# Kernel tuning notes

Measured on AMD Instinct MI355X. Metric: run time of the kernel, lower is better.

Reference implementation:

```python
import jax, jax.numpy as jnp
import numpy as np

H = 2048            # hidden_size
IN = 64             # input_size
EMB = 8             # EMBEDDING_DIMS
LIN = IN - 4 + 4 * EMB  # 92, LSTM input width
NH = 13             # number of prediction heads
MAXO = 9            # max head output width (gear)
HEAD_OUTS = [5, 1, 1, 1, 1, 1, 1, 1, 9, 1, 3, 1, 1]
LN_EPS = 1e-5


def setup_inputs() -> dict:
    key = jax.random.key(0)
    ks = jax.random.split(key, 22)
    s = 1.0 / np.sqrt(H)
    d = {}
    d["lap_cont"] = jax.random.normal(ks[0], (1, 1, IN - 4), jnp.float32)
    d["idx"] = jax.random.randint(ks[1], (1, 1, 4), 0, 5)  # compound, driver, track, team
    d["h_s"] = 0.1 * jax.random.normal(ks[2], (2, 1, H), jnp.float32)
    d["c_s"] = 0.1 * jax.random.normal(ks[3], (2, 1, H), jnp.float32)
    d["emb_team"] = 0.02 * jax.random.normal(ks[4], (10, EMB), jnp.float32)
    d["emb_track"] = 0.02 * jax.random.normal(ks[5], (48, EMB), jnp.float32)
    d["emb_driver"] = 0.02 * jax.random.normal(ks[6], (46, EMB), jnp.float32)
    d["emb_compound"] = 0.02 * jax.random.normal(ks[7], (5, EMB), jnp.float32)
    d["W_ih0"] = s * jax.random.normal(ks[8], (4 * H, LIN), jnp.float32)
    d["W_hh0"] = s * jax.random.normal(ks[9], (4 * H, H), jnp.float32)
    d["b_ih0"] = s * jax.random.normal(ks[10], (4 * H,), jnp.float32)
    d["b_hh0"] = s * jax.random.normal(ks[11], (4 * H,), jnp.float32)
    d["W_ih1"] = s * jax.random.normal(ks[12], (4 * H, H), jnp.float32)
    d["W_hh1"] = s * jax.random.normal(ks[13], (4 * H, H), jnp.float32)
    d["b_ih1"] = s * jax.random.normal(ks[14], (4 * H,), jnp.float32)
    d["b_hh1"] = s * jax.random.normal(ks[15], (4 * H,), jnp.float32)
    d["ln_g"] = jnp.ones((H,), jnp.float32)
    d["ln_b"] = jnp.zeros((H,), jnp.float32)
    d["head_W1"] = 0.02 * jax.random.normal(ks[16], (NH, 64, H), jnp.float32)
    d["head_b1"] = 0.02 * jax.random.normal(ks[17], (NH, 64), jnp.float32)
    d["head_W2"] = 0.02 * jax.random.normal(ks[18], (NH, MAXO, 64), jnp.float32)  # padded to MAXO
    d["head_b2"] = 0.02 * jax.random.normal(ks[19], (NH, MAXO), jnp.float32)
    return d


def _lstm_cell(x, h, c, Wih, Whh, bih, bhh):
    # x:[1,in], h,c:[1,H]; PyTorch gate order i,f,g,o
    g = x @ Wih.T + bih + h @ Whh.T + bhh
    i, f, gg, o = jnp.split(g, 4, axis=-1)
    c_new = jax.nn.sigmoid(f) * c + jax.nn.sigmoid(i) * jnp.tanh(gg)
    h_new = jax.nn.sigmoid(o) * jnp.tanh(c_new)
    return h_new, c_new


def reference(lap_cont, idx, h_s, c_s, emb_team, emb_track, emb_driver, emb_compound,
              W_ih0, W_hh0, b_ih0, b_hh0, W_ih1, W_hh1, b_ih1, b_hh1,
              ln_g, ln_b, head_W1, head_b1, head_W2, head_b2):
    # Embeddings (idx order: compound, driver, track_status, team)
    comp_e = emb_compound[idx[:, :, 0]]
    drv_e = emb_driver[idx[:, :, 1]]
    trk_e = emb_track[idx[:, :, 2]]
    team_e = emb_team[idx[:, :, 3]]
    x = jnp.concatenate([lap_cont, team_e, trk_e, drv_e, comp_e], axis=-1)  # [1,1,LIN]

    x2 = x[0]  # seq_len=1 -> single cell step; [1,LIN]
    h0, c0 = _lstm_cell(x2, h_s[0], c_s[0], W_ih0, W_hh0, b_ih0, b_hh0)
    h1, c1 = _lstm_cell(h0, h_s[1], c_s[1], W_ih1, W_hh1, b_ih1, b_hh1)
    new_h = jnp.stack([h0, h1], axis=0)
    new_c = jnp.stack([c0, c1], axis=0)

    h_t = h1[None]  # [1,1,H]
    mu = jnp.mean(h_t, axis=-1, keepdims=True)
    var = jnp.mean(jnp.square(h_t - mu), axis=-1, keepdims=True)
    h_t = (h_t - mu) * jax.lax.rsqrt(var + LN_EPS) * ln_g + ln_b

    # All 13 heads fused: Dropout is identity at inference
    hid = jax.nn.relu(jnp.einsum('bsh,koh->bsko', h_t, head_W1) + head_b1)  # [1,1,13,64]
    outs = jnp.einsum('bsko,kpo->bskp', hid, head_W2) + head_b2              # [1,1,13,9]

    heads = [outs[:, :, k, :HEAD_OUTS[k]] for k in range(NH)]
    return (new_h, new_c, *heads)
```

## Files before the change

### kernel.cpp

```cpp
#include <hip/hip_runtime.h>
#include <hip/hip_bf16.h>

#define H 2048
#define LIN 92

typedef __hip_bfloat16 bf16;

__device__ __align__(16) float g_x[96];
__device__ __align__(16) float g_hs[2][H];
__device__ __align__(16) float g_cs[2][H];
__device__ __align__(16) float g_p1[4 * H];
__device__ __align__(16) float g_h0[H];
__device__ __align__(16) float g_h1[H];
__device__ __align__(16) float g_ht[H];
__device__ __align__(16) float g_hid[13 * 64];

__device__ __forceinline__ float b2f(bf16 v) { return __bfloat162float(v); }
__device__ __forceinline__ float sg(float x) { return 1.f / (1.f + __expf(-x)); }

__device__ __forceinline__ bool is_bf16(const void* ln_g) {
    return *reinterpret_cast<const unsigned*>(ln_g) == 0x3F803F80u;
}

__device__ __forceinline__ float ld(const void* p, long i, bool bf) {
    return bf ? b2f(((const bf16*)p)[i]) : ((const float*)p)[i];
}

struct F8 { float v[8]; };

__device__ __forceinline__ F8 load8bf(const bf16* p) {
    uint4 u = *reinterpret_cast<const uint4*>(p);
    F8 r;
    r.v[0] = __uint_as_float(u.x << 16); r.v[1] = __uint_as_float(u.x & 0xffff0000u);
    r.v[2] = __uint_as_float(u.y << 16); r.v[3] = __uint_as_float(u.y & 0xffff0000u);
    r.v[4] = __uint_as_float(u.z << 16); r.v[5] = __uint_as_float(u.z & 0xffff0000u);
    r.v[6] = __uint_as_float(u.w << 16); r.v[7] = __uint_as_float(u.w & 0xffff0000u);
    return r;
}

__device__ __forceinline__ float wred(float x) {
    #pragma unroll
    for (int o = 32; o > 0; o >>= 1) x += __shfl_down(x, o);
    return x;
}

__device__ __forceinline__ float dotw(const void* W, long rowoff, const float* vec,
                                      int lane, bool bf) {
    float acc = 0.f;
    if (bf) {
        const bf16* r = (const bf16*)W + rowoff;
        #pragma unroll
        for (int i = 0; i < 4; i++) {
            int col = i * 512 + lane * 8;
            F8 a = load8bf(r + col);
            const float4* hp = reinterpret_cast<const float4*>(vec + col);
            float4 h0 = hp[0], h1 = hp[1];
            acc = fmaf(a.v[0], h0.x, acc); acc = fmaf(a.v[1], h0.y, acc);
            acc = fmaf(a.v[2], h0.z, acc); acc = fmaf(a.v[3], h0.w, acc);
            acc = fmaf(a.v[4], h1.x, acc); acc = fmaf(a.v[5], h1.y, acc);
            acc = fmaf(a.v[6], h1.z, acc); acc = fmaf(a.v[7], h1.w, acc);
        }
    } else {
        const float* r = (const float*)W + rowoff;
        #pragma unroll
        for (int i = 0; i < 4; i++) {
            int col = i * 512 + lane * 8;
            const float4* ap = reinterpret_cast<const float4*>(r + col);
            const float4* hp = reinterpret_cast<const float4*>(vec + col);
            float4 a0 = ap[0], a1 = ap[1];
            float4 h0 = hp[0], h1 = hp[1];
            acc = fmaf(a0.x, h0.x, acc); acc = fmaf(a0.y, h0.y, acc);
            acc = fmaf(a0.z, h0.z, acc); acc = fmaf(a0.w, h0.w, acc);
            acc = fmaf(a1.x, h1.x, acc); acc = fmaf(a1.y, h1.y, acc);
            acc = fmaf(a1.z, h1.z, acc); acc = fmaf(a1.w, h1.w, acc);
        }
    }
    return acc;
}

__global__ __launch_bounds__(256) void k_prep(
    const void* __restrict__ lap, const int* __restrict__ idx,
    const void* __restrict__ h_s, const void* __restrict__ c_s,
    const void* __restrict__ e_team, const void* __restrict__ e_trk,
    const void* __restrict__ e_drv, const void* __restrict__ e_cmp,
    const void* __restrict__ ln_g)
{
    bool bf = is_bf16(ln_g);
    int tid = threadIdx.x;
    for (int i = tid; i < H; i += 256) {
        g_hs[0][i] = ld(h_s, i, bf);
        g_hs[1][i] = ld(h_s, H + i, bf);
        g_cs[0][i] = ld(c_s, i, bf);
        g_cs[1][i] = ld(c_s, H + i, bf);
    }
    if (tid < LIN) {
        float v;
        if (tid < 60)      v = ld(lap, tid, bf);
        else if (tid < 68) v = ld(e_team, idx[3] * 8 + tid - 60, bf);
        else if (tid < 76) v = ld(e_trk,  idx[2] * 8 + tid - 68, bf);
        else if (tid < 84) v = ld(e_drv,  idx[1] * 8 + tid - 76, bf);
        else               v = ld(e_cmp,  idx[0] * 8 + tid - 84, bf);
        g_x[tid] = v;
    }
}

__global__ __launch_bounds__(256) void k_phaseA(
    const void* __restrict__ Wih0, const void* __restrict__ Whh0,
    const void* __restrict__ bih0, const void* __restrict__ bhh0,
    const void* __restrict__ Whh1, const void* __restrict__ bih1,
    const void* __restrict__ bhh1, const void* __restrict__ ln_g,
    float* __restrict__ out)
{
    bool bf = is_bf16(ln_g);
    int tid = threadIdx.x, w = tid >> 6, lane = tid & 63;
    if (blockIdx.x < H) {
        int j = blockIdx.x;
        __shared__ float gsh[4];
        long row = j + (long)w * H;
        float acc = 0.f;
        if (lane < 46) {
            long o = row * LIN + lane * 2;
            acc = g_x[lane * 2] * ld(Wih0, o, bf) + g_x[lane * 2 + 1] * ld(Wih0, o + 1, bf);
        }
        acc += dotw(Whh0, row * H, g_hs[0], lane, bf);
        acc = wred(acc);
        if (lane == 0) gsh[w] = acc + ld(bih0, row, bf) + ld(bhh0, row, bf);
        __syncthreads();
        if (tid == 0) {
            float gi = gsh[0], gf = gsh[1], gg = gsh[2], go = gsh[3];
            float cp = g_cs[0][j];
            float cn = sg(gf) * cp + sg(gi) * tanhf(gg);
            float hn = sg(go) * tanhf(cn);
            out[j]         = hn;
            out[2 * H + j] = cn;
            g_h0[j] = hn;
        }
    } else {
        long row = (long)(blockIdx.x - H) * 4 + w;
        float acc = dotw(Whh1, row * H, g_hs[1], lane, bf);
        acc = wred(acc);
        if (lane == 0) g_p1[row] = acc + ld(bih1, row, bf) + ld(bhh1, row, bf);
    }
}

__global__ __launch_bounds__(256) void k_lstm1(
    const void* __restrict__ Wih1, const void* __restrict__ ln_g,
    float* __restrict__ out)
{
    bool bf = is_bf16(ln_g);
    int tid = threadIdx.x, w = tid >> 6, lane = tid & 63;
    int j = blockIdx.x;
    long row = j + (long)w * H;
    float acc = dotw(Wih1, row * H, g_h0, lane, bf);
    acc = wred(acc);
    __shared__ float gsh[4];
    if (lane == 0) gsh[w] = acc + g_p1[row];
    __syncthreads();
    if (tid == 0) {
        float gi = gsh[0], gf = gsh[1], gg = gsh[2], go = gsh[3];
        float cp = g_cs[1][j];
        float cn = sg(gf) * cp + sg(gi) * tanhf(gg);
        float hn = sg(go) * tanhf(cn);
        out[H + j]     = hn;
        out[3 * H + j] = cn;
        g_h1[j] = hn;
    }
}

__global__ __launch_bounds__(256) void k_ln(
    const void* __restrict__ g, const void* __restrict__ b)
{
    bool bf = is_bf16(g);
    int tid = threadIdx.x, w = tid >> 6, lane = tid & 63;
    float vals[8];
    float s = 0.f, s2 = 0.f;
    #pragma unroll
    for (int i = 0; i < 8; i++) {
        float v = g_h1[tid + i * 256];
        vals[i] = v; s += v; s2 += v * v;
    }
    s = wred(s); s2 = wred(s2);
    __shared__ float sh[8];
    __shared__ float mv[2];
    if (lane == 0) { sh[w] = s; sh[4 + w] = s2; }
    __syncthreads();
    if (tid == 0) {
        float ts = sh[0] + sh[1] + sh[2] + sh[3];
        float t2 = sh[4] + sh[5] + sh[6] + sh[7];
        float mu = ts / (float)H;
        float var = t2 / (float)H - mu * mu;
        mv[0] = mu; mv[1] = rsqrtf(var + 1e-5f);
    }
    __syncthreads();
    float mu = mv[0], rs = mv[1];
    #pragma unroll
    for (int i = 0; i < 8; i++) {
        int e = tid + i * 256;
        g_ht[e] = (vals[i] - mu) * rs * ld(g, e, bf) + ld(b, e, bf);
    }
}

__global__ __launch_bounds__(256) void k_head1(
    const void* __restrict__ W1, const void* __restrict__ b1,
    const void* __restrict__ ln_g)
{
    bool bf = is_bf16(ln_g);
    int tid = threadIdx.x, w = tid >> 6, lane = tid & 63;
    int k = blockIdx.x >> 4, o = (blockIdx.x & 15) * 4 + w;
    float acc = dotw(W1, ((long)k * 64 + o) * H, g_ht, lane, bf);
    acc = wred(acc);
    if (lane == 0) {
        float v = acc + ld(b1, k * 64 + o, bf);
        g_hid[k * 64 + o] = v > 0.f ? v : 0.f;
    }
}

__global__ __launch_bounds__(128) void k_head2(
    const void* __restrict__ W2, const void* __restrict__ b2,
    const void* __restrict__ ln_g, float* __restrict__ out)
{
    const int HO[13]  = {5,1,1,1,1,1,1,1,9,1,3,1,1};
    const int OFF[13] = {0,5,6,7,8,9,10,11,12,21,22,25,26};
    bool bf = is_bf16(ln_g);
    int t = threadIdx.x;
    if (t >= 117) return;
    int k = t / 9, p = t % 9;
    if (p >= HO[k]) return;
    long wbase = ((long)k * 9 + p) * 64;
    const float* hp = g_hid + k * 64;
    float acc = ld(b2, k * 9 + p, bf);
    #pragma unroll
    for (int o = 0; o < 64; o++) acc = fmaf(hp[o], ld(W2, wbase + o, bf), acc);
    out[4 * H + OFF[k] + p] = acc;
}

extern "C" void kernel_launch(void* const* d_in, const int* in_sizes, int n_in,
                              void* d_out, int out_size, void* d_ws, size_t ws_size,
                              hipStream_t stream) {
    const void* lap    = d_in[0];
    const int*  idx    = (const int*)d_in[1];
    const void* h_s    = d_in[2];
    const void* c_s    = d_in[3];
    const void* e_team = d_in[4];
    const void* e_trk  = d_in[5];
    const void* e_drv  = d_in[6];
    const void* e_cmp  = d_in[7];
    const void* Wih0   = d_in[8];
    const void* Whh0   = d_in[9];
    const void* bih0   = d_in[10];
    const void* bhh0   = d_in[11];
    const void* Wih1   = d_in[12];
    const void* Whh1   = d_in[13];
    const void* bih1   = d_in[14];
    const void* bhh1   = d_in[15];
    const void* ln_g   = d_in[16];
    const void* ln_b   = d_in[17];
    const void* hW1    = d_in[18];
    const void* hb1    = d_in[19];
    const void* hW2    = d_in[20];
    const void* hb2    = d_in[21];
    float* out = (float*)d_out;

    k_prep<<<1, 256, 0, stream>>>(lap, idx, h_s, c_s, e_team, e_trk, e_drv, e_cmp, ln_g);
    k_phaseA<<<4096, 256, 0, stream>>>(Wih0, Whh0, bih0, bhh0, Whh1, bih1, bhh1, ln_g, out);
    k_lstm1<<<2048, 256, 0, stream>>>(Wih1, ln_g, out);
    k_ln<<<1, 256, 0, stream>>>(ln_g, ln_b);
    k_head1<<<208, 256, 0, stream>>>(hW1, hb1, ln_g);
    k_head2<<<1, 128, 0, stream>>>(hW2, hb2, ln_g, out);
}
```

Baseline: 267.9 us.

## Fuse prep into LSTM kernels, stage vectors in LDS, drop bf16 path

Removes the runtime bf16/fp32 dispatch and hardcodes fp32. The prep kernel is folded into the first LSTM kernel, with h_s and x staged in shared memory, and each warp now computes four rows. Fewer, larger blocks give more per-wave memory parallelism. LayerNorm is fused into the head1 kernel, with each block recomputing LN redundantly, which cuts launch count from six to four. In exchange, bf16 inputs are no longer supported.

```diff
diff --git a/kernel.cpp b/kernel.cpp
--- a/kernel.cpp
+++ b/kernel.cpp
@@ -1,42 +1,13 @@
 #include <hip/hip_runtime.h>
-#include <hip/hip_bf16.h>
 
 #define H 2048
-#define LIN 92
-
-typedef __hip_bfloat16 bf16;
-
-__device__ __align__(16) float g_x[96];
-__device__ __align__(16) float g_hs[2][H];
-__device__ __align__(16) float g_cs[2][H];
+
 __device__ __align__(16) float g_p1[4 * H];
 __device__ __align__(16) float g_h0[H];
 __device__ __align__(16) float g_h1[H];
-__device__ __align__(16) float g_ht[H];
 __device__ __align__(16) float g_hid[13 * 64];
 
-__device__ __forceinline__ float b2f(bf16 v) { return __bfloat162float(v); }
 __device__ __forceinline__ float sg(float x) { return 1.f / (1.f + __expf(-x)); }
-
-__device__ __forceinline__ bool is_bf16(const void* ln_g) {
-    return *reinterpret_cast<const unsigned*>(ln_g) == 0x3F803F80u;
-}
-
-__device__ __forceinline__ float ld(const void* p, long i, bool bf) {
-    return bf ? b2f(((const bf16*)p)[i]) : ((const float*)p)[i];
-}
-
-struct F8 { float v[8]; };
-
-__device__ __forceinline__ F8 load8bf(const bf16* p) {
-    uint4 u = *reinterpret_cast<const uint4*>(p);
-    F8 r;
-    r.v[0] = __uint_as_float(u.x << 16); r.v[1] = __uint_as_float(u.x & 0xffff0000u);
-    r.v[2] = __uint_as_float(u.y << 16); r.v[3] = __uint_as_float(u.y & 0xffff0000u);
-    r.v[4] = __uint_as_float(u.z << 16); r.v[5] = __uint_as_float(u.z & 0xffff0000u);
-    r.v[6] = __uint_as_float(u.w << 16); r.v[7] = __uint_as_float(u.w & 0xffff0000u);
-    return r;
-}
 
 __device__ __forceinline__ float wred(float x) {
     #pragma unroll
@@ -44,91 +15,69 @@
     return x;
 }
 
-__device__ __forceinline__ float dotw(const void* W, long rowoff, const float* vec,
-                                      int lane, bool bf) {
+__device__ __forceinline__ float dotg(const float* __restrict__ row,
+                                      const float* __restrict__ vec, int lane) {
     float acc = 0.f;
-    if (bf) {
-        const bf16* r = (const bf16*)W + rowoff;
-        #pragma unroll
-        for (int i = 0; i < 4; i++) {
-            int col = i * 512 + lane * 8;
-            F8 a = load8bf(r + col);
-            const float4* hp = reinterpret_cast<const float4*>(vec + col);
-            float4 h0 = hp[0], h1 = hp[1];
-            acc = fmaf(a.v[0], h0.x, acc); acc = fmaf(a.v[1], h0.y, acc);
-            acc = fmaf(a.v[2], h0.z, acc); acc = fmaf(a.v[3], h0.w, acc);
-            acc = fmaf(a.v[4], h1.x, acc); acc = fmaf(a.v[5], h1.y, acc);
-            acc = fmaf(a.v[6], h1.z, acc); acc = fmaf(a.v[7], h1.w, acc);
-        }
-    } else {
-        const float* r = (const float*)W + rowoff;
-        #pragma unroll
-        for (int i = 0; i < 4; i++) {
-            int col = i * 512 + lane * 8;
-            const float4* ap = reinterpret_cast<const float4*>(r + col);
-            const float4* hp = reinterpret_cast<const float4*>(vec + col);
-            float4 a0 = ap[0], a1 = ap[1];
-            float4 h0 = hp[0], h1 = hp[1];
-            acc = fmaf(a0.x, h0.x, acc); acc = fmaf(a0.y, h0.y, acc);
-            acc = fmaf(a0.z, h0.z, acc); acc = fmaf(a0.w, h0.w, acc);
-            acc = fmaf(a1.x, h1.x, acc); acc = fmaf(a1.y, h1.y, acc);
-            acc = fmaf(a1.z, h1.z, acc); acc = fmaf(a1.w, h1.w, acc);
-        }
+    #pragma unroll
+    for (int i = 0; i < 8; i++) {
+        int c = i * 256 + lane * 4;
+        float4 a = *reinterpret_cast<const float4*>(row + c);
+        float4 v = *reinterpret_cast<const float4*>(vec + c);
+        acc = fmaf(a.x, v.x, acc); acc = fmaf(a.y, v.y, acc);
+        acc = fmaf(a.z, v.z, acc); acc = fmaf(a.w, v.w, acc);
     }
     return acc;
 }
 
-__global__ __launch_bounds__(256) void k_prep(
-    const void* __restrict__ lap, const int* __restrict__ idx,
-    const void* __restrict__ h_s, const void* __restrict__ c_s,
-    const void* __restrict__ e_team, const void* __restrict__ e_trk,
-    const void* __restrict__ e_drv, const void* __restrict__ e_cmp,
-    const void* __restrict__ ln_g)
-{
-    bool bf = is_bf16(ln_g);
-    int tid = threadIdx.x;
-    for (int i = tid; i < H; i += 256) {
-        g_hs[0][i] = ld(h_s, i, bf);
-        g_hs[1][i] = ld(h_s, H + i, bf);
-        g_cs[0][i] = ld(c_s, i, bf);
-        g_cs[1][i] = ld(c_s, H + i, bf);
-    }
-    if (tid < LIN) {
+__global__ __launch_bounds__(256) void k1(
+    const float* __restrict__ lap, const int* __restrict__ idx,
+    const float* __restrict__ h_s, const float* __restrict__ c_s,
+    const float* __restrict__ e_team, const float* __restrict__ e_trk,
+    const float* __restrict__ e_drv, const float* __restrict__ e_cmp,
+    const float* __restrict__ Wih0, const float* __restrict__ Whh0,
+    const float* __restrict__ bih0, const float* __restrict__ bhh0,
+    const float* __restrict__ Whh1, const float* __restrict__ bih1,
+    const float* __restrict__ bhh1, float* __restrict__ out)
+{
+    __shared__ float vec[H];
+    __shared__ float xsh[96];
+    int tid = threadIdx.x, w = tid >> 6, lane = tid & 63;
+    int b = blockIdx.x;
+    bool l0 = b < 512;
+    const float* src = l0 ? h_s : (h_s + H);
+    #pragma unroll
+    for (int i = 0; i < 8; i++) vec[tid + i * 256] = src[tid + i * 256];
+    if (l0 && tid < 92) {
         float v;
-        if (tid < 60)      v = ld(lap, tid, bf);
-        else if (tid < 68) v = ld(e_team, idx[3] * 8 + tid - 60, bf);
-        else if (tid < 76) v = ld(e_trk,  idx[2] * 8 + tid - 68, bf);
-        else if (tid < 84) v = ld(e_drv,  idx[1] * 8 + tid - 76, bf);
-        else               v = ld(e_cmp,  idx[0] * 8 + tid - 84, bf);
-        g_x[tid] = v;
-    }
-}
-
-__global__ __launch_bounds__(256) void k_phaseA(
-    const void* __restrict__ Wih0, const void* __restrict__ Whh0,
-    const void* __restrict__ bih0, const void* __restrict__ bhh0,
-    const void* __restrict__ Whh1, const void* __restrict__ bih1,
-    const void* __restrict__ bhh1, const void* __restrict__ ln_g,
-    float* __restrict__ out)
-{
-    bool bf = is_bf16(ln_g);
-    int tid = threadIdx.x, w = tid >> 6, lane = tid & 63;
-    if (blockIdx.x < H) {
-        int j = blockIdx.x;
-        __shared__ float gsh[4];
-        long row = j + (long)w * H;
-        float acc = 0.f;
-        if (lane < 46) {
-            long o = row * LIN + lane * 2;
-            acc = g_x[lane * 2] * ld(Wih0, o, bf) + g_x[lane * 2 + 1] * ld(Wih0, o + 1, bf);
-        }
-        acc += dotw(Whh0, row * H, g_hs[0], lane, bf);
-        acc = wred(acc);
-        if (lane == 0) gsh[w] = acc + ld(bih0, row, bf) + ld(bhh0, row, bf);
-        __syncthreads();
-        if (tid == 0) {
-            float gi = gsh[0], gf = gsh[1], gg = gsh[2], go = gsh[3];
-            float cp = g_cs[0][j];
+        if (tid < 60)      v = lap[tid];
+        else if (tid < 68) v = e_team[idx[3] * 8 + tid - 60];
+        else if (tid < 76) v = e_trk [idx[2] * 8 + tid - 68];
+        else if (tid < 84) v = e_drv [idx[1] * 8 + tid - 76];
+        else               v = e_cmp [idx[0] * 8 + tid - 84];
+        xsh[tid] = v;
+    }
+    __syncthreads();
+
+    if (l0) {
+        int j = b * 4 + w;
+        float acc[4];
+        #pragma unroll
+        for (int g = 0; g < 4; g++) {
+            long row = j + (long)g * H;
+            float a = dotg(Whh0 + row * H, vec, lane);
+            const float* wr = Wih0 + row * 92;
+            float p = xsh[lane] * wr[lane];
+            if (lane < 28) p += xsh[lane + 64] * wr[lane + 64];
+            acc[g] = a + p;
+        }
+        #pragma unroll
+        for (int g = 0; g < 4; g++) acc[g] = wred(acc[g]);
+        if (lane == 0) {
+            float gi = acc[0] + bih0[j]         + bhh0[j];
+            float gf = acc[1] + bih0[j + H]     + bhh0[j + H];
+            float gg = acc[2] + bih0[j + 2 * H] + bhh0[j + 2 * H];
+            float go = acc[3] + bih0[j + 3 * H] + bhh0[j + 3 * H];
+            float cp = c_s[j];
             float cn = sg(gf) * cp + sg(gi) * tanhf(gg);
             float hn = sg(go) * tanhf(cn);
             out[j]         = hn;
@@ -136,29 +85,40 @@
             g_h0[j] = hn;
         }
     } else {
-        long row = (long)(blockIdx.x - H) * 4 + w;
-        float acc = dotw(Whh1, row * H, g_hs[1], lane, bf);
-        acc = wred(acc);
-        if (lane == 0) g_p1[row] = acc + ld(bih1, row, bf) + ld(bhh1, row, bf);
-    }
-}
-
-__global__ __launch_bounds__(256) void k_lstm1(
-    const void* __restrict__ Wih1, const void* __restrict__ ln_g,
+        int rb = (b - 512) * 16 + w * 4;
+        float acc[4];
+        #pragma unroll
+        for (int r = 0; r < 4; r++) acc[r] = dotg(Whh1 + (long)(rb + r) * H, vec, lane);
+        #pragma unroll
+        for (int r = 0; r < 4; r++) acc[r] = wred(acc[r]);
+        if (lane == 0) {
+            #pragma unroll
+            for (int r = 0; r < 4; r++) g_p1[rb + r] = acc[r] + bih1[rb + r] + bhh1[rb + r];
+        }
+    }
+}
+
+__global__ __launch_bounds__(256) void k2(
+    const float* __restrict__ Wih1, const float* __restrict__ c_s,
     float* __restrict__ out)
 {
-    bool bf = is_bf16(ln_g);
+    __shared__ float vec[H];
     int tid = threadIdx.x, w = tid >> 6, lane = tid & 63;
-    int j = blockIdx.x;
-    long row = j + (long)w * H;
-    float acc = dotw(Wih1, row * H, g_h0, lane, bf);
-    acc = wred(acc);
-    __shared__ float gsh[4];
-    if (lane == 0) gsh[w] = acc + g_p1[row];
-    __syncthreads();
-    if (tid == 0) {
-        float gi = gsh[0], gf = gsh[1], gg = gsh[2], go = gsh[3];
-        float cp = g_cs[1][j];
+    #pragma unroll
+    for (int i = 0; i < 8; i++) vec[tid + i * 256] = g_h0[tid + i * 256];
+    __syncthreads();
+    int j = blockIdx.x * 4 + w;
+    float acc[4];
+    #pragma unroll
+    for (int g = 0; g < 4; g++) acc[g] = dotg(Wih1 + (long)(j + g * H) * H, vec, lane);
+    #pragma unroll
+    for (int g = 0; g < 4; g++) acc[g] = wred(acc[g]);
+    if (lane == 0) {
+        float gi = acc[0] + g_p1[j];
+        float gf = acc[1] + g_p1[j + H];
+        float gg = acc[2] + g_p1[j + 2 * H];
+        float go = acc[3] + g_p1[j + 3 * H];
+        float cp = c_s[H + j];
         float cn = sg(gf) * cp + sg(gi) * tanhf(gg);
         float hn = sg(go) * tanhf(cn);
         out[H + j]     = hn;
@@ -167,104 +127,101 @@
     }
 }
 
-__global__ __launch_bounds__(256) void k_ln(
-    const void* __restrict__ g, const void* __restrict__ b)
-{
-    bool bf = is_bf16(g);
+__global__ __launch_bounds__(256) void k3(
+    const float* __restrict__ ln_g, const float* __restrict__ ln_b,
+    const float* __restrict__ W1, const float* __restrict__ b1)
+{
+    __shared__ float ht[H];
+    __shared__ float red[8];
+    __shared__ float mvs[2];
     int tid = threadIdx.x, w = tid >> 6, lane = tid & 63;
-    float vals[8];
+    float v[8];
     float s = 0.f, s2 = 0.f;
     #pragma unroll
     for (int i = 0; i < 8; i++) {
-        float v = g_h1[tid + i * 256];
-        vals[i] = v; s += v; s2 += v * v;
+        float x = g_h1[tid + i * 256];
+        v[i] = x; s += x; s2 += x * x;
     }
     s = wred(s); s2 = wred(s2);
-    __shared__ float sh[8];
-    __shared__ float mv[2];
-    if (lane == 0) { sh[w] = s; sh[4 + w] = s2; }
+    if (lane == 0) { red[w] = s; red[4 + w] = s2; }
     __syncthreads();
     if (tid == 0) {
-        float ts = sh[0] + sh[1] + sh[2] + sh[3];
-        float t2 = sh[4] + sh[5] + sh[6] + sh[7];
+        float ts = red[0] + red[1] + red[2] + red[3];
+        float t2 = red[4] + red[5] + red[6] + red[7];
         float mu = ts / (float)H;
         float var = t2 / (float)H - mu * mu;
-        mv[0] = mu; mv[1] = rsqrtf(var + 1e-5f);
-    }
-    __syncthreads();
-    float mu = mv[0], rs = mv[1];
+        mvs[0] = mu; mvs[1] = rsqrtf(var + 1e-5f);
+    }
+    __syncthreads();
+    float mu = mvs[0], rs = mvs[1];
     #pragma unroll
     for (int i = 0; i < 8; i++) {
         int e = tid + i * 256;
-        g_ht[e] = (vals[i] - mu) * rs * ld(g, e, bf) + ld(b, e, bf);
-    }
-}
-
-__global__ __launch_bounds__(256) void k_head1(
-    const void* __restrict__ W1, const void* __restrict__ b1,
-    const void* __restrict__ ln_g)
-{
-    bool bf = is_bf16(ln_g);
-    int tid = threadIdx.x, w = tid >> 6, lane = tid & 63;
-    int k = blockIdx.x >> 4, o = (blockIdx.x & 15) * 4 + w;
-    float acc = dotw(W1, ((long)k * 64 + o) * H, g_ht, lane, bf);
-    acc = wred(acc);
-    if (lane == 0) {
-        float v = acc + ld(b1, k * 64 + o, bf);
-        g_hid[k * 64 + o] = v > 0.f ? v : 0.f;
-    }
-}
-
-__global__ __launch_bounds__(128) void k_head2(
-    const void* __restrict__ W2, const void* __restrict__ b2,
-    const void* __restrict__ ln_g, float* __restrict__ out)
+        ht[e] = (v[i] - mu) * rs * ln_g[e] + ln_b[e];
+    }
+    __syncthreads();
+    int k  = blockIdx.x >> 3;
+    int u0 = (blockIdx.x & 7) * 8 + w * 2;
+    #pragma unroll
+    for (int u = 0; u < 2; u++) {
+        int o = u0 + u;
+        float acc = dotg(W1 + ((long)k * 64 + o) * H, ht, lane);
+        acc = wred(acc);
+        if (lane == 0) {
+            float r = acc + b1[k * 64 + o];
+            g_hid[k * 64 + o] = r > 0.f ? r : 0.f;
+        }
+    }
+}
+
+__global__ __launch_bounds__(128) void k4(
+    const float* __restrict__ W2, const float* __restrict__ b2,
+    float* __restrict__ out)
 {
     const int HO[13]  = {5,1,1,1,1,1,1,1,9,1,3,1,1};
     const int OFF[13] = {0,5,6,7,8,9,10,11,12,21,22,25,26};
-    bool bf = is_bf16(ln_g);
     int t = threadIdx.x;
     if (t >= 117) return;
     int k = t / 9, p = t % 9;
     if (p >= HO[k]) return;
-    long wbase = ((long)k * 9 + p) * 64;
+    const float* wr = W2 + ((long)k * 9 + p) * 64;
     const float* hp = g_hid + k * 64;
-    float acc = ld(b2, k * 9 + p, bf);
-    #pragma unroll
-    for (int o = 0; o < 64; o++) acc = fmaf(hp[o], ld(W2, wbase + o, bf), acc);
+    float acc = b2[k * 9 + p];
+    #pragma unroll
+    for (int o = 0; o < 64; o++) acc = fmaf(hp[o], wr[o], acc);
     out[4 * H + OFF[k] + p] = acc;
 }
 
 extern "C" void kernel_launch(void* const* d_in, const int* in_sizes, int n_in,
                               void* d_out, int out_size, void* d_ws, size_t ws_size,
                               hipStream_t stream) {
-    const void* lap    = d_in[0];
-    const int*  idx    = (const int*)d_in[1];
-    const void* h_s    = d_in[2];
-    const void* c_s    = d_in[3];
-    const void* e_team = d_in[4];
-    const void* e_trk  = d_in[5];
-    const void* e_drv  = d_in[6];
-    const void* e_cmp  = d_in[7];
-    const void* Wih0   = d_in[8];
-    const void* Whh0   = d_in[9];
-    const void* bih0   = d_in[10];
-    const void* bhh0   = d_in[11];
-    const void* Wih1   = d_in[12];
-    const void* Whh1   = d_in[13];
-    const void* bih1   = d_in[14];
-    const void* bhh1   = d_in[15];
-    const void* ln_g   = d_in[16];
-    const void* ln_b   = d_in[17];
-    const void* hW1    = d_in[18];
-    const void* hb1    = d_in[19];
-    const void* hW2    = d_in[20];
-    const void* hb2    = d_in[21];
+    const float* lap    = (const float*)d_in[0];
+    const int*   idx    = (const int*)  d_in[1];
+    const float* h_s    = (const float*)d_in[2];
+    const float* c_s    = (const float*)d_in[3];
+    const float* e_team = (const float*)d_in[4];
+    const float* e_trk  = (const float*)d_in[5];
+    const float* e_drv  = (const float*)d_in[6];
+    const float* e_cmp  = (const float*)d_in[7];
+    const float* Wih0   = (const float*)d_in[8];
+    const float* Whh0   = (const float*)d_in[9];
+    const float* bih0   = (const float*)d_in[10];
+    const float* bhh0   = (const float*)d_in[11];
+    const float* Wih1   = (const float*)d_in[12];
+    const float* Whh1   = (const float*)d_in[13];
+    const float* bih1   = (const float*)d_in[14];
+    const float* bhh1   = (const float*)d_in[15];
+    const float* ln_g   = (const float*)d_in[16];
+    const float* ln_b   = (const float*)d_in[17];
+    const float* hW1    = (const float*)d_in[18];
+    const float* hb1    = (const float*)d_in[19];
+    const float* hW2    = (const float*)d_in[20];
+    const float* hb2    = (const float*)d_in[21];
     float* out = (float*)d_out;
 
-    k_prep<<<1, 256, 0, stream>>>(lap, idx, h_s, c_s, e_team, e_trk, e_drv, e_cmp, ln_g);
-    k_phaseA<<<4096, 256, 0, stream>>>(Wih0, Whh0, bih0, bhh0, Whh1, bih1, bhh1, ln_g, out);
-    k_lstm1<<<2048, 256, 0, stream>>>(Wih1, ln_g, out);
-    k_ln<<<1, 256, 0, stream>>>(ln_g, ln_b);
-    k_head1<<<208, 256, 0, stream>>>(hW1, hb1, ln_g);
-    k_head2<<<1, 128, 0, stream>>>(hW2, hb2, ln_g, out);
-}
+    k1<<<1024, 256, 0, stream>>>(lap, idx, h_s, c_s, e_team, e_trk, e_drv, e_cmp,
+                                 Wih0, Whh0, bih0, bhh0, Whh1, bih1, bhh1, out);
+    k2<<<512, 256, 0, stream>>>(Wih1, c_s, out);
+    k3<<<104, 256, 0, stream>>>(ln_g, ln_b, hW1, hb1);
+    k4<<<1, 128, 0, stream>>>(hW2, hb2, out);
+}
```

Result: faster. 249.8 us (-6.8%).
